# Kernel tuning notes

Measured on AMD Instinct MI355X. Metric: run time of the kernel, lower is better.

Reference implementation:

```python
import jax, jax.numpy as jnp
import numpy as np

B, C = 16384, 4096

def setup_inputs() -> dict:
    key = jax.random.key(0)
    k1, k2 = jax.random.split(key)
    output = jax.random.normal(k1, (B, C), dtype=jnp.float32)
    target = jax.random.randint(k2, (B, C), 0, 2, dtype=jnp.int32)  # multi-hot 0/1
    return {"output": output, "target": target}

def reference(output, target):
    # softmax over class dim (dim=1 in torch)
    p = jax.nn.softmax(output, axis=1)  # [B, C]
    # loss[b] = log(sum_n exp(p[b,n])) - sum_{n: target[b,n]==1} p[b,n]
    lse = jax.scipy.special.logsumexp(p, axis=1)              # [B]
    masked = jnp.sum(p * (target == 1).astype(p.dtype), axis=1)  # [B]
    loss = lse - masked
    return jnp.mean(loss)
```

## Files before the change

kernel.cpp:

```cpp
#include <hip/hip_runtime.h>

constexpr int C_CLS = 4096;
constexpr int BLOCK = 256;
constexpr int WAVES = BLOCK / 64;
constexpr int LANE_V4 = C_CLS / (64 * 4);
constexpr int CHUNK = 4;

typedef float v4f __attribute__((ext_vector_type(4)));
typedef int v4i __attribute__((ext_vector_type(4)));

__device__ inline float wave_reduce_sum(float v) {
#pragma unroll
    for (int off = 32; off > 0; off >>= 1) v += __shfl_down(v, off, 64);
    return v;
}

template <bool ATOMIC>
__global__ __launch_bounds__(BLOCK) void ce_row_kernel(const float* __restrict__ x,
                                                       const int* __restrict__ tgt,
                                                       float* __restrict__ dst,
                                                       float inv_b, int nrows) {
    const int lane = threadIdx.x & 63;
    const int wave = threadIdx.x >> 6;
    const int row = blockIdx.x * WAVES + wave;
    if (row >= nrows) return;

    const v4f* xr = reinterpret_cast<const v4f*>(x + (size_t)row * C_CLS);
    const v4i* tr = reinterpret_cast<const v4i*>(tgt + (size_t)row * C_CLS);

    float s1 = 0.f, s2 = 0.f, s3 = 0.f, sm = 0.f;
#pragma unroll 1
    for (int c = 0; c < LANE_V4; c += CHUNK) {
        v4f xv[CHUNK];
        v4i tv[CHUNK];
#pragma unroll
        for (int i = 0; i < CHUNK; ++i)
            xv[i] = __builtin_nontemporal_load(&xr[lane + (c + i) * 64]);
#pragma unroll
        for (int i = 0; i < CHUNK; ++i)
            tv[i] = __builtin_nontemporal_load(&tr[lane + (c + i) * 64]);
#pragma unroll
        for (int i = 0; i < CHUNK; ++i) {
            const float e0 = __expf(xv[i].x);
            const float e1 = __expf(xv[i].y);
            const float e2 = __expf(xv[i].z);
            const float e3 = __expf(xv[i].w);
            s1 += (e0 + e1) + (e2 + e3);
            const float q0 = e0 * e0, q1 = e1 * e1, q2 = e2 * e2, q3 = e3 * e3;
            s2 += (q0 + q1) + (q2 + q3);
            s3 += (q0 * e0 + q1 * e1) + (q2 * e2 + q3 * e3);
            sm += (float)tv[i].x * e0 + (float)tv[i].y * e1 +
                  (float)tv[i].z * e2 + (float)tv[i].w * e3;
        }
    }

    s1 = wave_reduce_sum(s1);
    s2 = wave_reduce_sum(s2);
    s3 = wave_reduce_sum(s3);
    sm = wave_reduce_sum(sm);

    if (lane == 0) {
        const float inv = 1.f / s1;
        const float sum_exp_p = (float)C_CLS + 1.f +
                                inv * inv * (0.5f * s2 + 0.16666667f * inv * s3);
        const float loss = __logf(sum_exp_p) - sm * inv;
        if (ATOMIC) {
            atomicAdd(dst, loss * inv_b);
        } else {
            dst[row] = loss;
        }
    }
}

__global__ __launch_bounds__(BLOCK) void ce_reduce_kernel(const float* __restrict__ rl,
                                                          float* __restrict__ out,
                                                          int n4, float inv_b) {
    const v4f* r4 = reinterpret_cast<const v4f*>(rl);
    float s = 0.f;
    for (int i = threadIdx.x; i < n4; i += BLOCK) {
        const v4f v = r4[i];
        s += (v.x + v.y) + (v.z + v.w);
    }
    s = wave_reduce_sum(s);
    __shared__ float sh[WAVES];
    const int lane = threadIdx.x & 63;
    const int wave = threadIdx.x >> 6;
    if (lane == 0) sh[wave] = s;
    __syncthreads();
    if (threadIdx.x == 0) out[0] = ((sh[0] + sh[1]) + (sh[2] + sh[3])) * inv_b;
}

__global__ void ce_zero_kernel(float* out) { out[0] = 0.f; }

extern "C" void kernel_launch(void* const* d_in, const int* in_sizes, int n_in,
                              void* d_out, int out_size, void* d_ws, size_t ws_size,
                              hipStream_t stream) {
    const float* x = (const float*)d_in[0];
    const int* tgt = (const int*)d_in[1];
    float* out = (float*)d_out;

    const int B = in_sizes[0] / C_CLS;
    const float inv_b = 1.0f / (float)B;
    const int grid = (B + WAVES - 1) / WAVES;

    if (ws_size >= (size_t)B * sizeof(float)) {
        float* row_loss = (float*)d_ws;
        ce_row_kernel<false><<<grid, BLOCK, 0, stream>>>(x, tgt, row_loss, inv_b, B);
        ce_reduce_kernel<<<1, BLOCK, 0, stream>>>(row_loss, out, B / 4, inv_b);
    } else {
        ce_zero_kernel<<<1, 1, 0, stream>>>(out);
        ce_row_kernel<true><<<grid, BLOCK, 0, stream>>>(x, tgt, out, inv_b, B);
    }
}
```

Measured before the change: 473.6 us.

## Split target bit-packing into separate kernel and software-pipeline the x pass

Adds a pre-pass kernel that packs the int32 multi-hot target into a 64-bit mask per lane (8 MiB), then a second kernel streams x with double-buffered loads and applies the mask via bit tests. The aim is to decouple the two input streams and overlap loads with exp math. Total DRAM traffic still includes reading the full int target once plus a mask write and read, so bytes moved increase slightly. It also adds an extra kernel launch and needs a larger workspace, falling back to the old path otherwise.

```diff
diff --git a/kernel.cpp b/kernel.cpp
--- a/kernel.cpp
+++ b/kernel.cpp
@@ -4,15 +4,107 @@
 constexpr int BLOCK = 256;
 constexpr int WAVES = BLOCK / 64;
 constexpr int LANE_V4 = C_CLS / (64 * 4);
-constexpr int CHUNK = 4;
+constexpr int CHUNK = 2;
+constexpr int NCH = LANE_V4 / CHUNK;
 
 typedef float v4f __attribute__((ext_vector_type(4)));
 typedef int v4i __attribute__((ext_vector_type(4)));
+typedef unsigned long long u64;
 
 __device__ inline float wave_reduce_sum(float v) {
 #pragma unroll
     for (int off = 32; off > 0; off >>= 1) v += __shfl_down(v, off, 64);
     return v;
+}
+
+__global__ __launch_bounds__(BLOCK) void ce_pack_kernel(const int* __restrict__ tgt,
+                                                        u64* __restrict__ msk,
+                                                        int nrows) {
+    const int lane = threadIdx.x & 63;
+    const int wave = threadIdx.x >> 6;
+    const int row = blockIdx.x * WAVES + wave;
+    if (row >= nrows) return;
+
+    const v4i* tr = reinterpret_cast<const v4i*>(tgt + (size_t)row * C_CLS);
+    u64 m = 0;
+#pragma unroll
+    for (int c = 0; c < LANE_V4; ++c) {
+        const v4i t = __builtin_nontemporal_load(&tr[lane + c * 64]);
+        const unsigned nib = (t.x & 1) | ((t.y & 1) << 1) |
+                             ((t.z & 1) << 2) | ((t.w & 1) << 3);
+        m |= (u64)nib << (4 * c);
+    }
+    msk[(size_t)row * 64 + lane] = m;
+}
+
+template <bool ATOMIC>
+__global__ __launch_bounds__(BLOCK) void ce_x_kernel(const float* __restrict__ x,
+                                                     const u64* __restrict__ msk,
+                                                     float* __restrict__ dst,
+                                                     float inv_b, int nrows) {
+    const int lane = threadIdx.x & 63;
+    const int wave = threadIdx.x >> 6;
+    const int row = blockIdx.x * WAVES + wave;
+    if (row >= nrows) return;
+
+    const v4f* xr = reinterpret_cast<const v4f*>(x + (size_t)row * C_CLS);
+    const u64 m = msk[(size_t)row * 64 + lane];
+
+    float s1 = 0.f, s2 = 0.f, s3 = 0.f, sm = 0.f;
+    v4f xa[CHUNK], xb[CHUNK];
+
+    auto load_chunk = [&](v4f* xv, int ch) {
+        const int base = lane + ch * CHUNK * 64;
+#pragma unroll
+        for (int i = 0; i < CHUNK; ++i)
+            xv[i] = __builtin_nontemporal_load(&xr[base + i * 64]);
+    };
+
+    auto consume = [&](const v4f* xv, int ch) {
+#pragma unroll
+        for (int i = 0; i < CHUNK; ++i) {
+            const float e0 = __expf(xv[i].x);
+            const float e1 = __expf(xv[i].y);
+            const float e2 = __expf(xv[i].z);
+            const float e3 = __expf(xv[i].w);
+            s1 += (e0 + e1) + (e2 + e3);
+            const float q0 = e0 * e0, q1 = e1 * e1, q2 = e2 * e2, q3 = e3 * e3;
+            s2 += (q0 + q1) + (q2 + q3);
+            s3 += (q0 * e0 + q1 * e1) + (q2 * e2 + q3 * e3);
+            const unsigned nib = (unsigned)(m >> (4 * (ch * CHUNK + i))) & 0xFu;
+            sm += ((nib & 1u) ? e0 : 0.f) + ((nib & 2u) ? e1 : 0.f) +
+                  ((nib & 4u) ? e2 : 0.f) + ((nib & 8u) ? e3 : 0.f);
+        }
+    };
+
+    load_chunk(xa, 0);
+#pragma unroll 1
+    for (int c = 0; c < NCH - 2; c += 2) {
+        load_chunk(xb, c + 1);
+        consume(xa, c);
+        load_chunk(xa, c + 2);
+        consume(xb, c + 1);
+    }
+    load_chunk(xb, NCH - 1);
+    consume(xa, NCH - 2);
+    consume(xb, NCH - 1);
+
+    s1 = wave_reduce_sum(s1);
+    s2 = wave_reduce_sum(s2);
+    s3 = wave_reduce_sum(s3);
+    sm = wave_reduce_sum(sm);
+
+    if (lane == 0) {
+        const float inv = 1.f / s1;
+        const float sum_exp_p = (float)C_CLS + 1.f +
+                                inv * inv * (0.5f * s2 + 0.16666667f * inv * s3);
+        const float loss = __logf(sum_exp_p) - sm * inv;
+        if (ATOMIC) {
+            atomicAdd(dst, loss * inv_b);
+        } else {
+            dst[row] = loss;
+        }
+    }
 }
 
 template <bool ATOMIC>
@@ -30,17 +122,17 @@
 
     float s1 = 0.f, s2 = 0.f, s3 = 0.f, sm = 0.f;
 #pragma unroll 1
-    for (int c = 0; c < LANE_V4; c += CHUNK) {
-        v4f xv[CHUNK];
-        v4i tv[CHUNK];
-#pragma unroll
-        for (int i = 0; i < CHUNK; ++i)
+    for (int c = 0; c < LANE_V4; c += 4) {
+        v4f xv[4];
+        v4i tv[4];
+#pragma unroll
+        for (int i = 0; i < 4; ++i)
             xv[i] = __builtin_nontemporal_load(&xr[lane + (c + i) * 64]);
 #pragma unroll
-        for (int i = 0; i < CHUNK; ++i)
+        for (int i = 0; i < 4; ++i)
             tv[i] = __builtin_nontemporal_load(&tr[lane + (c + i) * 64]);
 #pragma unroll
-        for (int i = 0; i < CHUNK; ++i) {
+        for (int i = 0; i < 4; ++i) {
             const float e0 = __expf(xv[i].x);
             const float e1 = __expf(xv[i].y);
             const float e2 = __expf(xv[i].z);
@@ -103,7 +195,16 @@
     const float inv_b = 1.0f / (float)B;
     const int grid = (B + WAVES - 1) / WAVES;
 
-    if (ws_size >= (size_t)B * sizeof(float)) {
+    const size_t mask_bytes = (size_t)B * 64 * sizeof(u64);
+    const size_t rl_bytes = (size_t)B * sizeof(float);
+
+    if (ws_size >= mask_bytes + rl_bytes) {
+        u64* masks = (u64*)d_ws;
+        float* row_loss = (float*)((char*)d_ws + mask_bytes);
+        ce_pack_kernel<<<grid, BLOCK, 0, stream>>>(tgt, masks, B);
+        ce_x_kernel<false><<<grid, BLOCK, 0, stream>>>(x, masks, row_loss, inv_b, B);
+        ce_reduce_kernel<<<1, BLOCK, 0, stream>>>(row_loss, out, B / 4, inv_b);
+    } else if (ws_size >= rl_bytes) {
         float* row_loss = (float*)d_ws;
         ce_row_kernel<false><<<grid, BLOCK, 0, stream>>>(x, tgt, row_loss, inv_b, B);
         ce_reduce_kernel<<<1, BLOCK, 0, stream>>>(row_loss, out, B / 4, inv_b);
```

Result: no change. 482.5 us (+1.9%).

## Split rows into slices swept by a persistent grid with a finish kernel

Applied to the files above, without the earlier changes.

Replaces the one-wave-per-row kernel with a persistent grid-stride sweep in which each wave handles a 1 KB slice of a row. It software-prefetches the next slice and writes four partial moment sums per slice to workspace. A new finish kernel combines the 16 slices per row into row losses before the existing reduction. The goal is a more even, better-pipelined memory stream, at the cost of four wave reductions per slice, an extra kernel launch, and partial-sum traffic through workspace.

```diff
diff --git a/kernel.cpp b/kernel.cpp
--- a/kernel.cpp
+++ b/kernel.cpp
@@ -3,8 +3,12 @@
 constexpr int C_CLS = 4096;
 constexpr int BLOCK = 256;
 constexpr int WAVES = BLOCK / 64;
+constexpr int ROW_V4 = C_CLS / 4;
+constexpr int V4_PER_SLICE = 64;
+constexpr int SLICES_PER_ROW = ROW_V4 / V4_PER_SLICE;
+constexpr int GRID_SWEEP = 2048;
+constexpr int NWAVES = GRID_SWEEP * WAVES;
 constexpr int LANE_V4 = C_CLS / (64 * 4);
-constexpr int CHUNK = 4;
 
 typedef float v4f __attribute__((ext_vector_type(4)));
 typedef int v4i __attribute__((ext_vector_type(4)));
@@ -13,6 +17,81 @@
 #pragma unroll
     for (int off = 32; off > 0; off >>= 1) v += __shfl_down(v, off, 64);
     return v;
+}
+
+__global__ __launch_bounds__(BLOCK, 8) void ce_sweep_kernel(const float* __restrict__ x,
+                                                            const int* __restrict__ tgt,
+                                                            v4f* __restrict__ part,
+                                                            int nslices) {
+    const int lane = threadIdx.x & 63;
+    const int w = blockIdx.x * WAVES + (threadIdx.x >> 6);
+    const v4f* xv = reinterpret_cast<const v4f*>(x);
+    const v4i* tv = reinterpret_cast<const v4i*>(tgt);
+
+    int s = w;
+    if (s >= nslices) return;
+
+    v4f xa = __builtin_nontemporal_load(&xv[(size_t)s * 64 + lane]);
+    v4i ta = __builtin_nontemporal_load(&tv[(size_t)s * 64 + lane]);
+
+#pragma unroll 1
+    for (; s < nslices; s += NWAVES) {
+        const int sn = s + NWAVES;
+        v4f xb = {};
+        v4i tb = {};
+        if (sn < nslices) {
+            xb = __builtin_nontemporal_load(&xv[(size_t)sn * 64 + lane]);
+            tb = __builtin_nontemporal_load(&tv[(size_t)sn * 64 + lane]);
+        }
+
+        const float e0 = __expf(xa.x);
+        const float e1 = __expf(xa.y);
+        const float e2 = __expf(xa.z);
+        const float e3 = __expf(xa.w);
+        float s1 = (e0 + e1) + (e2 + e3);
+        const float q0 = e0 * e0, q1 = e1 * e1, q2 = e2 * e2, q3 = e3 * e3;
+        float s2 = (q0 + q1) + (q2 + q3);
+        float s3 = (q0 * e0 + q1 * e1) + (q2 * e2 + q3 * e3);
+        float sm = (float)ta.x * e0 + (float)ta.y * e1 +
+                   (float)ta.z * e2 + (float)ta.w * e3;
+
+        s1 = wave_reduce_sum(s1);
+        s2 = wave_reduce_sum(s2);
+        s3 = wave_reduce_sum(s3);
+        sm = wave_reduce_sum(sm);
+        if (lane == 0) {
+            v4f p;
+            p.x = s1; p.y = s2; p.z = s3; p.w = sm;
+            part[s] = p;
+        }
+
+        xa = xb;
+        ta = tb;
+    }
+}
+
+__global__ __launch_bounds__(BLOCK) void ce_finish_kernel(const v4f* __restrict__ part,
+                                                          float* __restrict__ row_loss,
+                                                          int nrows) {
+    const int lane = threadIdx.x & 63;
+    const int wv = threadIdx.x >> 6;
+    const int r0 = (blockIdx.x * WAVES + wv) * 4;
+    if (r0 >= nrows) return;
+
+    v4f p = part[(size_t)r0 * SLICES_PER_ROW + lane];
+#pragma unroll
+    for (int off = 8; off > 0; off >>= 1) {
+        p.x += __shfl_down(p.x, off, 16);
+        p.y += __shfl_down(p.y, off, 16);
+        p.z += __shfl_down(p.z, off, 16);
+        p.w += __shfl_down(p.w, off, 16);
+    }
+    if ((lane & 15) == 0) {
+        const float inv = 1.f / p.x;
+        const float sum_exp_p = (float)C_CLS + 1.f +
+                                inv * inv * (0.5f * p.y + 0.16666667f * inv * p.z);
+        row_loss[r0 + (lane >> 4)] = __logf(sum_exp_p) - p.w * inv;
+    }
 }
 
 template <bool ATOMIC>
@@ -30,17 +109,17 @@
 
     float s1 = 0.f, s2 = 0.f, s3 = 0.f, sm = 0.f;
 #pragma unroll 1
-    for (int c = 0; c < LANE_V4; c += CHUNK) {
-        v4f xv[CHUNK];
-        v4i tv[CHUNK];
-#pragma unroll
-        for (int i = 0; i < CHUNK; ++i)
+    for (int c = 0; c < LANE_V4; c += 4) {
+        v4f xv[4];
+        v4i tv[4];
+#pragma unroll
+        for (int i = 0; i < 4; ++i)
             xv[i] = __builtin_nontemporal_load(&xr[lane + (c + i) * 64]);
 #pragma unroll
-        for (int i = 0; i < CHUNK; ++i)
+        for (int i = 0; i < 4; ++i)
             tv[i] = __builtin_nontemporal_load(&tr[lane + (c + i) * 64]);
 #pragma unroll
-        for (int i = 0; i < CHUNK; ++i) {
+        for (int i = 0; i < 4; ++i) {
             const float e0 = __expf(xv[i].x);
             const float e1 = __expf(xv[i].y);
             const float e2 = __expf(xv[i].z);
@@ -101,14 +180,25 @@
 
     const int B = in_sizes[0] / C_CLS;
     const float inv_b = 1.0f / (float)B;
-    const int grid = (B + WAVES - 1) / WAVES;
-
-    if (ws_size >= (size_t)B * sizeof(float)) {
+    const int nslices = B * SLICES_PER_ROW;
+
+    const size_t part_bytes = (size_t)nslices * sizeof(v4f);
+    const size_t rl_bytes = (size_t)B * sizeof(float);
+
+    if (ws_size >= part_bytes + rl_bytes && (B % 16) == 0) {
+        v4f* part = (v4f*)d_ws;
+        float* row_loss = (float*)((char*)d_ws + part_bytes);
+        ce_sweep_kernel<<<GRID_SWEEP, BLOCK, 0, stream>>>(x, tgt, part, nslices);
+        ce_finish_kernel<<<B / 16, BLOCK, 0, stream>>>(part, row_loss, B);
+        ce_reduce_kernel<<<1, BLOCK, 0, stream>>>(row_loss, out, B / 4, inv_b);
+    } else if (ws_size >= rl_bytes) {
         float* row_loss = (float*)d_ws;
+        const int grid = (B + WAVES - 1) / WAVES;
         ce_row_kernel<false><<<grid, BLOCK, 0, stream>>>(x, tgt, row_loss, inv_b, B);
         ce_reduce_kernel<<<1, BLOCK, 0, stream>>>(row_loss, out, B / 4, inv_b);
     } else {
         ce_zero_kernel<<<1, 1, 0, stream>>>(out);
+        const int grid = (B + WAVES - 1) / WAVES;
         ce_row_kernel<true><<<grid, BLOCK, 0, stream>>>(x, tgt, out, inv_b, B);
     }
 }
```

Result: slower. 486.6 us (+2.7%).
